# Kernel optimization log

Hardware: AMD Instinct MI355X
Metric: run time of the kernel (lower is better)

Reference implementation:

```python
import jax, jax.numpy as jnp
import numpy as np

INPUT_CH = 32
INPUT_CH_VIEWS = 16
HIDDEN = 64
GEO_FEAT = 15
N_PTS = 2097152


def _kaiming(key, in_dim, out_dim):
    # mimic nn.Linear default init (kaiming uniform, fan_in)
    bound = 1.0 / np.sqrt(in_dim)
    return jax.random.uniform(key, (in_dim, out_dim), jnp.float32, -bound, bound)


def setup_inputs() -> dict:
    key = jax.random.key(0)
    ks = jax.random.split(key, 8)
    x = jax.random.normal(ks[0], (N_PTS, INPUT_CH + INPUT_CH_VIEWS), jnp.float32)
    # sigma net: 32 -> 64 -> 64 -> 16 (1 sigma + 15 geo feat), bias-free
    s0 = _kaiming(ks[1], INPUT_CH, HIDDEN)
    s1 = _kaiming(ks[2], HIDDEN, HIDDEN)
    s2 = _kaiming(ks[3], HIDDEN, 1 + GEO_FEAT)
    # color net: (16 views + 15 geo) = 31 -> 64 -> 64 -> 3, bias-free
    c0 = _kaiming(ks[4], INPUT_CH_VIEWS + GEO_FEAT, HIDDEN)
    c1 = _kaiming(ks[5], HIDDEN, HIDDEN)
    c2 = _kaiming(ks[6], HIDDEN, HIDDEN)
    c3 = _kaiming(ks[7], HIDDEN, 3)
    return {"x": x, "s0": s0, "s1": s1, "s2": s2,
            "c0": c0, "c1": c1, "c2": c2, "c3": c3}


def reference(x, s0, s1, s2, c0, c1, c2, c3):
    input_pts = x[..., :INPUT_CH]
    input_views = x[..., INPUT_CH:]
    # sigma net: ReLU between layers, no activation on last
    h = jax.nn.relu(input_pts @ s0)
    h = jax.nn.relu(h @ s1)
    h = h @ s2                      # [N, 1 + geo_feat]
    sigma = h[..., 0]
    geo_feat = h[..., 1:]
    # color net
    h = jnp.concatenate([input_views, geo_feat], axis=-1)
    h = jax.nn.relu(h @ c0)
    h = jax.nn.relu(h @ c1)
    h = jax.nn.relu(h @ c2)
    color = h @ c3                  # [N, 3]
    return jnp.concatenate([color, sigma[..., None]], axis=-1)  # [N, 4]
```

## Files before the change

kernel.cpp:

```cpp
#include <hip/hip_runtime.h>


typedef _Float16 half8  __attribute__((ext_vector_type(8)));
typedef float    floatx4 __attribute__((ext_vector_type(4)));

#define NPTS   2097152
#define NTILES (NPTS / 64)

__global__ void prep_weights(const float* __restrict__ ws0, const float* __restrict__ ws1,
                             const float* __restrict__ ws2, const float* __restrict__ wc0,
                             const float* __restrict__ wc1, const float* __restrict__ wc2,
                             const float* __restrict__ wc3, _Float16* __restrict__ wpack) {
    int t = blockIdx.x * blockDim.x + threadIdx.x;
    if (t >= 36 * 64) return;
    int fid = t >> 6, lane = t & 63, l16 = lane & 15, q = lane >> 4;
#pragma unroll
    for (int j = 0; j < 8; ++j) {
        int phi = (2 * 0 + (j >> 2)) * 16 + q * 4 + (j & 3);
        float v = 0.f;
        if (fid < 4) {
            v = ws0[(q * 8 + j) * 64 + fid * 16 + l16];
        } else if (fid < 12) {
            int mt = (fid - 4) >> 1, c = (fid - 4) & 1;
            int p = (2 * c + (j >> 2)) * 16 + q * 4 + (j & 3);
            v = ws1[p * 64 + mt * 16 + l16];
        } else if (fid < 14) {
            int c = fid - 12;
            int p = (2 * c + (j >> 2)) * 16 + q * 4 + (j & 3);
            v = ws2[p * 16 + l16];
        } else if (fid < 18) {
            int mt = fid - 14;
            if (j < 4) v = wc0[(q * 4 + j) * 64 + mt * 16 + l16];
            else {
                int g = q * 4 + (j - 4);
                v = (g == 0) ? 0.f : wc0[(15 + g) * 64 + mt * 16 + l16];
            }
        } else if (fid < 26) {
            int mt = (fid - 18) >> 1, c = (fid - 18) & 1;
            int p = (2 * c + (j >> 2)) * 16 + q * 4 + (j & 3);
            v = wc1[p * 64 + mt * 16 + l16];
        } else if (fid < 34) {
            int mt = (fid - 26) >> 1, c = (fid - 26) & 1;
            int p = (2 * c + (j >> 2)) * 16 + q * 4 + (j & 3);
            v = wc2[p * 64 + mt * 16 + l16];
        } else {
            int c = fid - 34;
            int p = (2 * c + (j >> 2)) * 16 + q * 4 + (j & 3);
            v = (l16 < 3) ? wc3[p * 3 + l16] : 0.f;
        }
        (void)phi;
        wpack[t * 8 + j] = (_Float16)v;
    }
}

__device__ __forceinline__ half8 packrelu(floatx4 a, floatx4 b) {
    half8 r;
    r[0] = (_Float16)fmaxf(a[0], 0.f); r[1] = (_Float16)fmaxf(a[1], 0.f);
    r[2] = (_Float16)fmaxf(a[2], 0.f); r[3] = (_Float16)fmaxf(a[3], 0.f);
    r[4] = (_Float16)fmaxf(b[0], 0.f); r[5] = (_Float16)fmaxf(b[1], 0.f);
    r[6] = (_Float16)fmaxf(b[2], 0.f); r[7] = (_Float16)fmaxf(b[3], 0.f);
    return r;
}

__global__ __launch_bounds__(256, 2)
void nerf_fused(const float* __restrict__ x, const _Float16* __restrict__ wpack,
                float* __restrict__ out) {
    const int lane = threadIdx.x & 63;
    const int w    = threadIdx.x >> 6;
    const int l16  = lane & 15;
    const int q    = lane >> 4;

    half8 W[36];
    const half8* wp = (const half8*)wpack;
#pragma unroll
    for (int f = 0; f < 36; ++f) W[f] = wp[f * 64 + lane];

    const floatx4 vz = {0.f, 0.f, 0.f, 0.f};
    const float4* xb = (const float4*)x;

    int tile = blockIdx.x;
    float4 vA, vB, vC;
    {
        size_t base = (size_t)(tile * 64 + w * 16 + l16) * 12;
        vA = xb[base + q * 2]; vB = xb[base + q * 2 + 1]; vC = xb[base + 8 + q];
    }

    while (tile < NTILES) {
        int next = tile + gridDim.x;
        int pf = next < NTILES ? next : tile;
        size_t nbase = (size_t)(pf * 64 + w * 16 + l16) * 12;
        float4 nA = xb[nbase + q * 2], nB = xb[nbase + q * 2 + 1], nC = xb[nbase + 8 + q];

        half8 b0, b1;
        b0[0] = (_Float16)vA.x; b0[1] = (_Float16)vA.y; b0[2] = (_Float16)vA.z; b0[3] = (_Float16)vA.w;
        b0[4] = (_Float16)vB.x; b0[5] = (_Float16)vB.y; b0[6] = (_Float16)vB.z; b0[7] = (_Float16)vB.w;
        floatx4 acc[4], a2[4];
#pragma unroll
        for (int mt = 0; mt < 4; ++mt)
            acc[mt] = __builtin_amdgcn_mfma_f32_16x16x32_f16(W[mt], b0, vz, 0, 0, 0);

        b0 = packrelu(acc[0], acc[1]); b1 = packrelu(acc[2], acc[3]);
#pragma unroll
        for (int mt = 0; mt < 4; ++mt) {
            a2[mt] = __builtin_amdgcn_mfma_f32_16x16x32_f16(W[4 + mt * 2], b0, vz,     0, 0, 0);
            a2[mt] = __builtin_amdgcn_mfma_f32_16x16x32_f16(W[5 + mt * 2], b1, a2[mt], 0, 0, 0);
        }

        b0 = packrelu(a2[0], a2[1]); b1 = packrelu(a2[2], a2[3]);
        floatx4 accS;
        accS = __builtin_amdgcn_mfma_f32_16x16x32_f16(W[12], b0, vz,   0, 0, 0);
        accS = __builtin_amdgcn_mfma_f32_16x16x32_f16(W[13], b1, accS, 0, 0, 0);
        float sigma = accS[0];

        half8 bc;
        bc[0] = (_Float16)vC.x; bc[1] = (_Float16)vC.y; bc[2] = (_Float16)vC.z; bc[3] = (_Float16)vC.w;
        bc[4] = (q == 0) ? (_Float16)0.f : (_Float16)accS[0];
        bc[5] = (_Float16)accS[1]; bc[6] = (_Float16)accS[2]; bc[7] = (_Float16)accS[3];
#pragma unroll
        for (int mt = 0; mt < 4; ++mt)
            acc[mt] = __builtin_amdgcn_mfma_f32_16x16x32_f16(W[14 + mt], bc, vz, 0, 0, 0);

        b0 = packrelu(acc[0], acc[1]); b1 = packrelu(acc[2], acc[3]);
#pragma unroll
        for (int mt = 0; mt < 4; ++mt) {
            a2[mt] = __builtin_amdgcn_mfma_f32_16x16x32_f16(W[18 + mt * 2], b0, vz,     0, 0, 0);
            a2[mt] = __builtin_amdgcn_mfma_f32_16x16x32_f16(W[19 + mt * 2], b1, a2[mt], 0, 0, 0);
        }

        b0 = packrelu(a2[0], a2[1]); b1 = packrelu(a2[2], a2[3]);
#pragma unroll
        for (int mt = 0; mt < 4; ++mt) {
            acc[mt] = __builtin_amdgcn_mfma_f32_16x16x32_f16(W[26 + mt * 2], b0, vz,      0, 0, 0);
            acc[mt] = __builtin_amdgcn_mfma_f32_16x16x32_f16(W[27 + mt * 2], b1, acc[mt], 0, 0, 0);
        }

        b0 = packrelu(acc[0], acc[1]); b1 = packrelu(acc[2], acc[3]);
        floatx4 accC;
        accC = __builtin_amdgcn_mfma_f32_16x16x32_f16(W[34], b0, vz,   0, 0, 0);
        accC = __builtin_amdgcn_mfma_f32_16x16x32_f16(W[35], b1, accC, 0, 0, 0);

        if (lane < 16) {
            float4 o;
            o.x = accC[0]; o.y = accC[1]; o.z = accC[2]; o.w = sigma;
            ((float4*)out)[(size_t)tile * 64 + w * 16 + lane] = o;
        }

        vA = nA; vB = nB; vC = nC;
        tile = next;
    }
}

extern "C" void kernel_launch(void* const* d_in, const int* in_sizes, int n_in,
                              void* d_out, int out_size, void* d_ws, size_t ws_size,
                              hipStream_t stream) {
    _Float16* wpack = (_Float16*)d_ws;
    prep_weights<<<9, 256, 0, stream>>>(
        (const float*)d_in[1], (const float*)d_in[2], (const float*)d_in[3],
        (const float*)d_in[4], (const float*)d_in[5], (const float*)d_in[6],
        (const float*)d_in[7], wpack);
    nerf_fused<<<1024, 256, 0, stream>>>((const float*)d_in[0], wpack, (float*)d_out);
}
```

Before: 549.3 us.

## Process two interleaved 16-point tiles per wave and defer next-chunk prefetch

Each wave now handles two independent 16-point sub-tiles per iteration, interleaving their MFMA chains so dependent matrix ops from one tile can overlap the other's latency. The prefetch of the next chunk's inputs moves to the middle of the loop to shorten live ranges of prefetch registers. Float-to-half conversions use packed round-toward-zero conversion intrinsics, which changes rounding mode slightly. Register pressure rises with doubled accumulators, which may hurt occupancy under the 2-block launch bound.

Result: no change. 557.4 us (+1.5%).

```diff
diff --git a/kernel.cpp b/kernel.cpp
--- a/kernel.cpp
+++ b/kernel.cpp
@@ -2,10 +2,11 @@
 
 
 typedef _Float16 half8  __attribute__((ext_vector_type(8)));
+typedef __fp16   pk16x2 __attribute__((ext_vector_type(2)));
 typedef float    floatx4 __attribute__((ext_vector_type(4)));
 
 #define NPTS   2097152
-#define NTILES (NPTS / 64)
+#define NCHUNK (NPTS / 128)
 
 __global__ void prep_weights(const float* __restrict__ ws0, const float* __restrict__ ws1,
                              const float* __restrict__ ws2, const float* __restrict__ wc0,
@@ -16,7 +17,6 @@
     int fid = t >> 6, lane = t & 63, l16 = lane & 15, q = lane >> 4;
 #pragma unroll
     for (int j = 0; j < 8; ++j) {
-        int phi = (2 * 0 + (j >> 2)) * 16 + q * 4 + (j & 3);
         float v = 0.f;
         if (fid < 4) {
             v = ws0[(q * 8 + j) * 64 + fid * 16 + l16];
@@ -48,17 +48,16 @@
             int p = (2 * c + (j >> 2)) * 16 + q * 4 + (j & 3);
             v = (l16 < 3) ? wc3[p * 3 + l16] : 0.f;
         }
-        (void)phi;
         wpack[t * 8 + j] = (_Float16)v;
     }
 }
 
 __device__ __forceinline__ half8 packrelu(floatx4 a, floatx4 b) {
-    half8 r;
-    r[0] = (_Float16)fmaxf(a[0], 0.f); r[1] = (_Float16)fmaxf(a[1], 0.f);
-    r[2] = (_Float16)fmaxf(a[2], 0.f); r[3] = (_Float16)fmaxf(a[3], 0.f);
-    r[4] = (_Float16)fmaxf(b[0], 0.f); r[5] = (_Float16)fmaxf(b[1], 0.f);
-    r[6] = (_Float16)fmaxf(b[2], 0.f); r[7] = (_Float16)fmaxf(b[3], 0.f);
+    half8 r; pk16x2 t;
+    t = __builtin_amdgcn_cvt_pkrtz(fmaxf(a[0], 0.f), fmaxf(a[1], 0.f)); r[0] = t[0]; r[1] = t[1];
+    t = __builtin_amdgcn_cvt_pkrtz(fmaxf(a[2], 0.f), fmaxf(a[3], 0.f)); r[2] = t[0]; r[3] = t[1];
+    t = __builtin_amdgcn_cvt_pkrtz(fmaxf(b[0], 0.f), fmaxf(b[1], 0.f)); r[4] = t[0]; r[5] = t[1];
+    t = __builtin_amdgcn_cvt_pkrtz(fmaxf(b[2], 0.f), fmaxf(b[3], 0.f)); r[6] = t[0]; r[7] = t[1];
     return r;
 }
 
@@ -78,75 +77,130 @@
     const floatx4 vz = {0.f, 0.f, 0.f, 0.f};
     const float4* xb = (const float4*)x;
 
-    int tile = blockIdx.x;
-    float4 vA, vB, vC;
-    {
-        size_t base = (size_t)(tile * 64 + w * 16 + l16) * 12;
-        vA = xb[base + q * 2]; vB = xb[base + q * 2 + 1]; vC = xb[base + 8 + q];
+    int chunk = blockIdx.x;
+    float4 vA[2], vB[2], vC[2];
+#pragma unroll
+    for (int u = 0; u < 2; ++u) {
+        size_t base = (size_t)(chunk * 128 + w * 32 + u * 16 + l16) * 12;
+        vA[u] = xb[base + q * 2]; vB[u] = xb[base + q * 2 + 1]; vC[u] = xb[base + 8 + q];
     }
 
-    while (tile < NTILES) {
-        int next = tile + gridDim.x;
-        int pf = next < NTILES ? next : tile;
-        size_t nbase = (size_t)(pf * 64 + w * 16 + l16) * 12;
-        float4 nA = xb[nbase + q * 2], nB = xb[nbase + q * 2 + 1], nC = xb[nbase + 8 + q];
-
-        half8 b0, b1;
-        b0[0] = (_Float16)vA.x; b0[1] = (_Float16)vA.y; b0[2] = (_Float16)vA.z; b0[3] = (_Float16)vA.w;
-        b0[4] = (_Float16)vB.x; b0[5] = (_Float16)vB.y; b0[6] = (_Float16)vB.z; b0[7] = (_Float16)vB.w;
-        floatx4 acc[4], a2[4];
-#pragma unroll
-        for (int mt = 0; mt < 4; ++mt)
-            acc[mt] = __builtin_amdgcn_mfma_f32_16x16x32_f16(W[mt], b0, vz, 0, 0, 0);
-
-        b0 = packrelu(acc[0], acc[1]); b1 = packrelu(acc[2], acc[3]);
-#pragma unroll
-        for (int mt = 0; mt < 4; ++mt) {
-            a2[mt] = __builtin_amdgcn_mfma_f32_16x16x32_f16(W[4 + mt * 2], b0, vz,     0, 0, 0);
-            a2[mt] = __builtin_amdgcn_mfma_f32_16x16x32_f16(W[5 + mt * 2], b1, a2[mt], 0, 0, 0);
-        }
-
-        b0 = packrelu(a2[0], a2[1]); b1 = packrelu(a2[2], a2[3]);
-        floatx4 accS;
-        accS = __builtin_amdgcn_mfma_f32_16x16x32_f16(W[12], b0, vz,   0, 0, 0);
-        accS = __builtin_amdgcn_mfma_f32_16x16x32_f16(W[13], b1, accS, 0, 0, 0);
-        float sigma = accS[0];
-
-        half8 bc;
-        bc[0] = (_Float16)vC.x; bc[1] = (_Float16)vC.y; bc[2] = (_Float16)vC.z; bc[3] = (_Float16)vC.w;
-        bc[4] = (q == 0) ? (_Float16)0.f : (_Float16)accS[0];
-        bc[5] = (_Float16)accS[1]; bc[6] = (_Float16)accS[2]; bc[7] = (_Float16)accS[3];
-#pragma unroll
-        for (int mt = 0; mt < 4; ++mt)
-            acc[mt] = __builtin_amdgcn_mfma_f32_16x16x32_f16(W[14 + mt], bc, vz, 0, 0, 0);
-
-        b0 = packrelu(acc[0], acc[1]); b1 = packrelu(acc[2], acc[3]);
-#pragma unroll
-        for (int mt = 0; mt < 4; ++mt) {
-            a2[mt] = __builtin_amdgcn_mfma_f32_16x16x32_f16(W[18 + mt * 2], b0, vz,     0, 0, 0);
-            a2[mt] = __builtin_amdgcn_mfma_f32_16x16x32_f16(W[19 + mt * 2], b1, a2[mt], 0, 0, 0);
-        }
-
-        b0 = packrelu(a2[0], a2[1]); b1 = packrelu(a2[2], a2[3]);
-#pragma unroll
-        for (int mt = 0; mt < 4; ++mt) {
-            acc[mt] = __builtin_amdgcn_mfma_f32_16x16x32_f16(W[26 + mt * 2], b0, vz,      0, 0, 0);
-            acc[mt] = __builtin_amdgcn_mfma_f32_16x16x32_f16(W[27 + mt * 2], b1, acc[mt], 0, 0, 0);
-        }
-
-        b0 = packrelu(acc[0], acc[1]); b1 = packrelu(acc[2], acc[3]);
-        floatx4 accC;
-        accC = __builtin_amdgcn_mfma_f32_16x16x32_f16(W[34], b0, vz,   0, 0, 0);
-        accC = __builtin_amdgcn_mfma_f32_16x16x32_f16(W[35], b1, accC, 0, 0, 0);
+    while (chunk < NCHUNK) {
+        int next = chunk + gridDim.x;
+        int pf = next < NCHUNK ? next : chunk;
+
+        half8 b0[2], b1[2];
+        floatx4 acc[2][4], a2[2][4];
+#pragma unroll
+        for (int u = 0; u < 2; ++u) {
+            pk16x2 t;
+            t = __builtin_amdgcn_cvt_pkrtz(vA[u].x, vA[u].y); b0[u][0] = t[0]; b0[u][1] = t[1];
+            t = __builtin_amdgcn_cvt_pkrtz(vA[u].z, vA[u].w); b0[u][2] = t[0]; b0[u][3] = t[1];
+            t = __builtin_amdgcn_cvt_pkrtz(vB[u].x, vB[u].y); b0[u][4] = t[0]; b0[u][5] = t[1];
+            t = __builtin_amdgcn_cvt_pkrtz(vB[u].z, vB[u].w); b0[u][6] = t[0]; b0[u][7] = t[1];
+        }
+#pragma unroll
+        for (int mt = 0; mt < 4; ++mt)
+#pragma unroll
+            for (int u = 0; u < 2; ++u)
+                acc[u][mt] = __builtin_amdgcn_mfma_f32_16x16x32_f16(W[mt], b0[u], vz, 0, 0, 0);
+
+#pragma unroll
+        for (int u = 0; u < 2; ++u) {
+            b0[u] = packrelu(acc[u][0], acc[u][1]);
+            b1[u] = packrelu(acc[u][2], acc[u][3]);
+        }
+#pragma unroll
+        for (int mt = 0; mt < 4; ++mt)
+#pragma unroll
+            for (int u = 0; u < 2; ++u) {
+                a2[u][mt] = __builtin_amdgcn_mfma_f32_16x16x32_f16(W[4 + mt * 2], b0[u], vz,        0, 0, 0);
+                a2[u][mt] = __builtin_amdgcn_mfma_f32_16x16x32_f16(W[5 + mt * 2], b1[u], a2[u][mt], 0, 0, 0);
+            }
+
+#pragma unroll
+        for (int u = 0; u < 2; ++u) {
+            b0[u] = packrelu(a2[u][0], a2[u][1]);
+            b1[u] = packrelu(a2[u][2], a2[u][3]);
+        }
+        floatx4 accS[2];
+        float sigma[2];
+#pragma unroll
+        for (int u = 0; u < 2; ++u) {
+            accS[u] = __builtin_amdgcn_mfma_f32_16x16x32_f16(W[12], b0[u], vz,      0, 0, 0);
+            accS[u] = __builtin_amdgcn_mfma_f32_16x16x32_f16(W[13], b1[u], accS[u], 0, 0, 0);
+        }
+
+#pragma unroll
+        for (int u = 0; u < 2; ++u) {
+            sigma[u] = accS[u][0];
+            pk16x2 t;
+            t = __builtin_amdgcn_cvt_pkrtz(vC[u].x, vC[u].y); b0[u][0] = t[0]; b0[u][1] = t[1];
+            t = __builtin_amdgcn_cvt_pkrtz(vC[u].z, vC[u].w); b0[u][2] = t[0]; b0[u][3] = t[1];
+            float g0 = (q == 0) ? 0.f : accS[u][0];
+            t = __builtin_amdgcn_cvt_pkrtz(g0, accS[u][1]);         b0[u][4] = t[0]; b0[u][5] = t[1];
+            t = __builtin_amdgcn_cvt_pkrtz(accS[u][2], accS[u][3]); b0[u][6] = t[0]; b0[u][7] = t[1];
+        }
+#pragma unroll
+        for (int mt = 0; mt < 4; ++mt)
+#pragma unroll
+            for (int u = 0; u < 2; ++u)
+                acc[u][mt] = __builtin_amdgcn_mfma_f32_16x16x32_f16(W[14 + mt], b0[u], vz, 0, 0, 0);
+
+#pragma unroll
+        for (int u = 0; u < 2; ++u) {
+            size_t nbase = (size_t)(pf * 128 + w * 32 + u * 16 + l16) * 12;
+            vA[u] = xb[nbase + q * 2]; vB[u] = xb[nbase + q * 2 + 1]; vC[u] = xb[nbase + 8 + q];
+        }
+
+#pragma unroll
+        for (int u = 0; u < 2; ++u) {
+            b0[u] = packrelu(acc[u][0], acc[u][1]);
+            b1[u] = packrelu(acc[u][2], acc[u][3]);
+        }
+#pragma unroll
+        for (int mt = 0; mt < 4; ++mt)
+#pragma unroll
+            for (int u = 0; u < 2; ++u) {
+                a2[u][mt] = __builtin_amdgcn_mfma_f32_16x16x32_f16(W[18 + mt * 2], b0[u], vz,        0, 0, 0);
+                a2[u][mt] = __builtin_amdgcn_mfma_f32_16x16x32_f16(W[19 + mt * 2], b1[u], a2[u][mt], 0, 0, 0);
+            }
+
+#pragma unroll
+        for (int u = 0; u < 2; ++u) {
+            b0[u] = packrelu(a2[u][0], a2[u][1]);
+            b1[u] = packrelu(a2[u][2], a2[u][3]);
+        }
+#pragma unroll
+        for (int mt = 0; mt < 4; ++mt)
+#pragma unroll
+            for (int u = 0; u < 2; ++u) {
+                acc[u][mt] = __builtin_amdgcn_mfma_f32_16x16x32_f16(W[26 + mt * 2], b0[u], vz,         0, 0, 0);
+                acc[u][mt] = __builtin_amdgcn_mfma_f32_16x16x32_f16(W[27 + mt * 2], b1[u], acc[u][mt], 0, 0, 0);
+            }
+
+#pragma unroll
+        for (int u = 0; u < 2; ++u) {
+            b0[u] = packrelu(acc[u][0], acc[u][1]);
+            b1[u] = packrelu(acc[u][2], acc[u][3]);
+        }
+        floatx4 accC[2];
+#pragma unroll
+        for (int u = 0; u < 2; ++u) {
+            accC[u] = __builtin_amdgcn_mfma_f32_16x16x32_f16(W[34], b0[u], vz,      0, 0, 0);
+            accC[u] = __builtin_amdgcn_mfma_f32_16x16x32_f16(W[35], b1[u], accC[u], 0, 0, 0);
+        }
 
         if (lane < 16) {
-            float4 o;
-            o.x = accC[0]; o.y = accC[1]; o.z = accC[2]; o.w = sigma;
-            ((float4*)out)[(size_t)tile * 64 + w * 16 + lane] = o;
-        }
-
-        vA = nA; vB = nB; vC = nC;
-        tile = next;
+#pragma unroll
+            for (int u = 0; u < 2; ++u) {
+                float4 o;
+                o.x = accC[u][0]; o.y = accC[u][1]; o.z = accC[u][2]; o.w = sigma[u];
+                ((float4*)out)[(size_t)chunk * 128 + w * 32 + u * 16 + lane] = o;
+            }
+        }
+
+        chunk = next;
     }
 }
 
```
